# Performance work log

Hardware: AMD Instinct MI355X
Metric: run time of the kernel (lower is better)

The kernel has to match this reference:

```python
import jax, jax.numpy as jnp
import numpy as np

# Static config (matches init_kwargs)
VOCAB, EMBED, HIDDEN = 32000, 256, 512
SLOTS, MEM_DIM, HEADS, TOPK = 1024, 64, 4, 8
B, T = 16, 128
# beta_read/beta_write are learned scalars but the torch forward detaches them
# via .item(); treat as constants (|beta| + 1e-6 with beta init ~1.0).
BETA_R = 1.0 + 1e-6
BETA_W = 1.0 + 1e-6
EPS = 1e-8


def setup_inputs() -> dict:
    key = jax.random.key(0)
    ks = jax.random.split(key, 16)
    s = 0.02
    HD = HEADS * MEM_DIM
    return {
        "input_seq": jax.random.randint(ks[0], (B, T), 0, VOCAB),
        "E": jax.random.normal(ks[1], (VOCAB, EMBED), jnp.float32) * s,
        "W_ih": jax.random.normal(ks[2], (4 * HIDDEN, EMBED + MEM_DIM), jnp.float32) * s,
        "W_hh": jax.random.normal(ks[3], (4 * HIDDEN, HIDDEN), jnp.float32) * s,
        "b_ih": jnp.zeros((4 * HIDDEN,), jnp.float32),
        "b_hh": jnp.zeros((4 * HIDDEN,), jnp.float32),
        "W_out": jax.random.normal(ks[4], (HIDDEN, VOCAB), jnp.float32) * s,
        "b_out": jnp.zeros((VOCAB,), jnp.float32),
        "W_rk": jax.random.normal(ks[5], (HIDDEN, HD), jnp.float32) * s,
        "b_rk": jnp.zeros((HD,), jnp.float32),
        "W_wk": jax.random.normal(ks[6], (HIDDEN, HD), jnp.float32) * s,
        "b_wk": jnp.zeros((HD,), jnp.float32),
        "W_wv": jax.random.normal(ks[7], (HIDDEN, HD), jnp.float32) * s,
        "b_wv": jnp.zeros((HD,), jnp.float32),
        "W_er": jax.random.normal(ks[8], (HIDDEN, HD), jnp.float32) * s,
        "b_er": jnp.zeros((HD,), jnp.float32),
    }


def _address(memory, keys, beta):
    # memory: [B,S,D], keys: [B,H,D] -> sparse (top-k) content weights [B,H,S]
    mem_n = memory / (jnp.linalg.norm(memory, axis=-1, keepdims=True) + EPS)
    key_n = keys / (jnp.linalg.norm(keys, axis=-1, keepdims=True) + EPS)
    scores = beta * jnp.einsum("bhd,bsd->bhs", key_n, mem_n)
    vals, idx = jax.lax.top_k(scores, TOPK)           # [B,H,K]
    sm = jax.nn.softmax(vals, axis=-1)                # softmax over top-k only
    w = jnp.zeros_like(scores)
    b_ix = jnp.arange(scores.shape[0])[:, None, None]
    h_ix = jnp.arange(HEADS)[None, :, None]
    return w.at[b_ix, h_ix, idx].set(sm)              # [B,H,S]


def reference(input_seq, E, W_ih, W_hh, b_ih, b_hh, W_out, b_out,
              W_rk, b_rk, W_wk, b_wk, W_wv, b_wv, W_er, b_er):
    Bq = input_seq.shape[0]
    memory0 = jnp.full((Bq, SLOTS, MEM_DIM), 1e-6, jnp.float32)
    h0 = jnp.zeros((Bq, HIDDEN), jnp.float32)
    c0 = jnp.zeros((Bq, HIDDEN), jnp.float32)
    r0 = jnp.zeros((Bq, MEM_DIM), jnp.float32)

    def step(carry, x_t):
        memory, h, c, read_vec = carry
        emb = E[x_t]                                          # [B,embed]
        inp = jnp.concatenate([emb, read_vec], axis=-1)
        gates = inp @ W_ih.T + b_ih + h @ W_hh.T + b_hh       # [B,4H]
        i, f, g, o = jnp.split(gates, 4, axis=-1)             # torch LSTM order
        c = jax.nn.sigmoid(f) * c + jax.nn.sigmoid(i) * jnp.tanh(g)
        h = jax.nn.sigmoid(o) * jnp.tanh(c)
        logits = h @ W_out + b_out                            # [B,V]
        rk = (h @ W_rk + b_rk).reshape(Bq, HEADS, MEM_DIM)
        wk = (h @ W_wk + b_wk).reshape(Bq, HEADS, MEM_DIM)
        wv = (h @ W_wv + b_wv).reshape(Bq, HEADS, MEM_DIM)
        er = jax.nn.sigmoid(h @ W_er + b_er).reshape(Bq, HEADS, MEM_DIM)
        # content-addressed top-k read
        rw = _address(memory, rk, BETA_R)                     # [B,H,S]
        read_vec = jnp.einsum("bhs,bsd->bhd", rw, memory).mean(axis=1)
        # erase + add write
        ww = _address(memory, wk, BETA_W)                     # [B,H,S]
        keep = jnp.prod(1.0 - ww[..., None] * er[:, :, None, :], axis=1)
        add = jnp.einsum("bhs,bhd->bsd", ww, wv)
        memory = memory * keep + add
        return (memory, h, c, read_vec), logits

    _, logits_seq = jax.lax.scan(step, (memory0, h0, c0, r0), input_seq.T)
    return jnp.transpose(logits_seq, (1, 0, 2))               # [B,T,V]
```

## Files before the change

### kernel.cpp

```cpp
#include <hip/hip_runtime.h>
#include <hip/hip_bf16.h>
#include <stdint.h>

typedef unsigned int uint;
typedef unsigned long long u64;

#define T_STEPS 128
#define BQ 16
#define HID 512
#define NSLOT 1024
#define MD 64
#define VOCAB 32000
#define BETA 1.000001f
#define EPSN 1e-8f

#define NWK 128
#define NBT 16

#define LF_FH(b)  ((b)*32)
#define LF_FP(w)  ((16+(w))*32)
#define LF_FC(w)  ((48+(w))*32)
#define LF_FRV(b) ((176+(b))*32)
#define LF_FG(w)  ((192+(w))*32)
#define NLINES    320

#define AL4(dst, p) asm volatile("global_load_dwordx4 %0, %1, off sc0 sc1" : "=v"(dst) : "v"(p))
#define ALF(dst, p) asm volatile("global_load_dword %0, %1, off sc0 sc1" : "=v"(dst) : "v"(p))
#define AWAIT() do { asm volatile("s_waitcnt vmcnt(0)" ::: "memory"); __builtin_amdgcn_sched_barrier(0); } while(0)
#define DRAIN() asm volatile("s_waitcnt vmcnt(0)" ::: "memory")

__device__ __forceinline__ float sigm(float x){ return 1.f/(1.f+expf(-x)); }
__device__ __forceinline__ void astoref(float* p, float v){
  __hip_atomic_store(p, v, __ATOMIC_RELAXED, __HIP_MEMORY_SCOPE_AGENT);
}
__device__ __forceinline__ void astoreu32(uint* p, uint v){
  __hip_atomic_store(p, v, __ATOMIC_RELAXED, __HIP_MEMORY_SCOPE_AGENT);
}
__device__ __forceinline__ void astoreu64(u64* p, u64 v){
  __hip_atomic_store(p, v, __ATOMIC_RELAXED, __HIP_MEMORY_SCOPE_AGENT);
}
__device__ __forceinline__ u64 aloadu64(const u64* p){
  return __hip_atomic_load((u64*)p, __ATOMIC_RELAXED, __HIP_MEMORY_SCOPE_AGENT);
}
__device__ __forceinline__ uint aloadu32(const uint* p){
  return __hip_atomic_load((uint*)p, __ATOMIC_RELAXED, __HIP_MEMORY_SCOPE_AGENT);
}
__device__ __forceinline__ void poll1(const uint* p, uint gen){
  while (aloadu32(p) < gen) __builtin_amdgcn_s_sleep(2);
}

__device__ __forceinline__ u64 packsc(float v, int slot){
  uint u = __float_as_uint(v);
  u = (u & 0x80000000u) ? ~u : (u | 0x80000000u);
  return ((u64)u << 10) | (u64)(1023 - slot);
}
__device__ __forceinline__ float unpackval(u64 p){
  uint u = (uint)(p >> 10);
  uint bits = (u & 0x80000000u) ? (u & 0x7fffffffu) : ~u;
  return __uint_as_float(bits);
}
__device__ __forceinline__ int unpackslot(u64 p){ return 1023 - (int)(p & 1023u); }

#define L_MEM  0
#define L_NRM  8704
#define L_HS   8832
#define L_KEY  17088
#define L_KNRM 17600
#define L_SC   17608
#define L_WV   18632
#define L_ER   18888
#define L_WL   19144
#define L_RVS  19208
#define L_WTS  20232
#define L_TOT  21256

__global__ __launch_bounds__(256) void prep_emb(const float* __restrict__ E,
                                                const int* __restrict__ seq,
                                                float* __restrict__ EMB){
  int m = blockIdx.x, t = m >> 4, b = m & 15;
  int x = seq[b*T_STEPS + t];
  EMB[(size_t)m*256 + threadIdx.x] = E[(size_t)x*256 + threadIdx.x];
}

__global__ __launch_bounds__(256) void gemm_emb(const float* __restrict__ A,
                                                const float* __restrict__ W_ih,
                                                const float* __restrict__ b_ih,
                                                const float* __restrict__ b_hh,
                                                float* __restrict__ C){
  __shared__ __align__(16) float As[16*68];
  __shared__ __align__(16) float Bs[16*68];
  int mt = blockIdx.x & 31, nt = blockIdx.x >> 5;
  int m0 = mt*64, n0 = nt*64;
  int tx = threadIdx.x & 15, ty = threadIdx.x >> 4;
  float acc[4][4] = {};
  for (int k0 = 0; k0 < 256; k0 += 16){
    int mm = threadIdx.x >> 2, kq = (threadIdx.x & 3)*4;
    float4 a = *(const float4*)(A + (size_t)(m0+mm)*256 + k0 + kq);
    As[(kq+0)*68+mm]=a.x; As[(kq+1)*68+mm]=a.y; As[(kq+2)*68+mm]=a.z; As[(kq+3)*68+mm]=a.w;
    int pp = n0 + mm;
    int r = (pp & 3)*512 + (pp >> 2);
    float4 bv = *(const float4*)(W_ih + (size_t)r*320 + k0 + kq);
    Bs[(kq+0)*68+mm]=bv.x; Bs[(kq+1)*68+mm]=bv.y; Bs[(kq+2)*68+mm]=bv.z; Bs[(kq+3)*68+mm]=bv.w;
    __syncthreads();
    #pragma unroll
    for (int kk = 0; kk < 16; ++kk){
      float4 av = *(const float4*)(As + kk*68 + ty*4);
      float4 bb = *(const float4*)(Bs + kk*68 + tx*4);
      float aa[4] = {av.x,av.y,av.z,av.w};
      float bv2[4] = {bb.x,bb.y,bb.z,bb.w};
      #pragma unroll
      for (int i = 0; i < 4; ++i)
        #pragma unroll
        for (int j = 0; j < 4; ++j)
          acc[i][j] = fmaf(aa[i], bv2[j], acc[i][j]);
    }
    __syncthreads();
  }
  #pragma unroll
  for (int i = 0; i < 4; ++i){
    int m = m0 + ty*4 + i;
    #pragma unroll
    for (int j = 0; j < 4; ++j){
      int pp = n0 + tx*4 + j;
      int r = (pp & 3)*512 + (pp >> 2);
      C[(size_t)m*2048 + pp] = acc[i][j] + b_ih[r] + b_hh[r];
    }
  }
}

__global__ __launch_bounds__(256) void make_wrvT(const float* __restrict__ W_ih,
                                                 float* __restrict__ WT){
  int idx = blockIdx.x*256 + threadIdx.x;
  int k = idx >> 11, p = idx & 2047;
  int r = (p & 3)*512 + (p >> 2);
  WT[idx] = W_ih[(size_t)r*320 + 256 + k];
}

__global__ __launch_bounds__(256) void recur_kernel(
    const float* __restrict__ W_hh, const float* __restrict__ WT,
    const float* __restrict__ W_rk, const float* __restrict__ b_rk,
    const float* __restrict__ W_wk, const float* __restrict__ b_wk,
    const float* __restrict__ W_wv, const float* __restrict__ b_wv,
    const float* __restrict__ W_er, const float* __restrict__ b_er,
    const float* __restrict__ G_emb, float* __restrict__ H_all,
    float* __restrict__ H_pub, float* __restrict__ mem_g,
    float* __restrict__ projpub, float* __restrict__ gatespub,
    float* __restrict__ rvpub, u64* __restrict__ cand,
    u64* __restrict__ wlist, uint* __restrict__ arrv)
{
  __shared__ __align__(16) float smem[L_TOT];
  const int tid = threadIdx.x;
  const int wg  = blockIdx.x;

  if (wg < NWK){
    float* mem_s  = smem + L_MEM;
    float* nrm_s  = smem + L_NRM;
    float* hs     = smem + L_HS;
    float* key_s  = smem + L_KEY;
    float* knrm_s = smem + L_KNRM;
    float* sc_s   = smem + L_SC;
    float* wv_s   = smem + L_WV;
    float* er_s   = smem + L_ER;
    u64*   wl_s   = (u64*)(smem + L_WL);
    float* rv_s   = smem + L_RVS;
    float* WT_s   = smem + L_WTS;

    const int b_s = wg >> 3, rg = wg & 7, s0 = rg*128;
    const int gb = tid >> 4, gc = tid & 15;
    const int pcol = wg*16 + gc;
    const int rrow = (pcol & 3)*512 + (pcol >> 2);
    float* mslice_g = mem_g + ((size_t)b_s*NSLOT + s0)*MD;
    const float* W1 = (wg < 16) ? W_rk : W_wk;
    const float* B1 = (wg < 16) ? b_rk : b_wk;
    const float* W2 = (wg < 16) ? W_wv : W_er;
    const float* B2 = (wg < 16) ? b_wv : b_er;
    const int cc = (wg & 15)*16 + gc;
    const float pb1 = (wg < 32) ? B1[cc] : 0.f;
    const float pb2 = (wg < 32) ? B2[cc] : 0.f;

    for (int i = tid; i < 64*16; i += 256){
      int d = i >> 4, c = i & 15;
      WT_s[i] = WT[(size_t)d*2048 + wg*16 + c];
    }
    for (int i = tid; i < 128*MD; i += 256){
      mem_s[(i >> 6)*68 + (i & 63)] = 1e-6f;
      astoref(mslice_g + i, 1e-6f);
    }
    __syncthreads();
    {
      int s = tid >> 1, half = tid & 1;
      const float4* mp = (const float4*)(mem_s + s*68 + half*32);
      float sum = 0.f;
      #pragma unroll
      for (int q = 0; q < 8; ++q){
        float4 v = mp[q];
        sum = fmaf(v.x,v.x,sum); sum = fmaf(v.y,v.y,sum);
        sum = fmaf(v.z,v.z,sum); sum = fmaf(v.w,v.w,sum);
      }
      sum += __shfl_xor(sum, 1);
      if (half == 0) nrm_s[s] = sqrtf(sum) + EPSN;
    }
    __syncthreads();

    #pragma clang loop unroll(disable)
    for (int t = 0; t < T_STEPS-1; ++t){
      const int par = t & 1, parp = par ^ 1;
      if (t > 0){
        if (tid < 32) wl_s[tid] = aloadu64(wlist + (size_t)b_s*32 + tid);
        if (tid < 64){
          float4 v; AL4(v, (const float4*)(projpub + (size_t)parp*BQ*1024 + (size_t)b_s*1024 + 512) + tid);
          AWAIT();
          *(float4*)(wv_s + tid*4) = v;
        } else if (tid < 128){
          int i = tid - 64;
          float4 v; AL4(v, (const float4*)(projpub + (size_t)parp*BQ*1024 + (size_t)b_s*1024 + 768) + i);
          AWAIT();
          *(float4*)(er_s + i*4) = v;
        }
        __syncthreads();
        if (tid < 64){
          const int d = tid;
          #pragma unroll 1
          for (int e = 0; e < 32; ++e){
            u64 w64 = wl_s[e];
            int sl = (int)(w64 & 0xffffffffu);
            if (sl >= s0 && sl < s0+128){
              float w = __uint_as_float((uint)(w64 >> 32));
              mem_s[(sl-s0)*68 + d] *= (1.f - w*er_s[(e >> 3)*64 + d]);
            }
          }
          #pragma unroll 1
          for (int e = 0; e < 32; ++e){
            u64 w64 = wl_s[e];
            int sl = (int)(w64 & 0xffffffffu);
            if (sl >= s0 && sl < s0+128){
              float w = __uint_as_float((uint)(w64 >> 32));
              mem_s[(sl-s0)*68 + d] += w*wv_s[(e >> 3)*64 + d];
            }
          }
          #pragma unroll 1
          for (int e = 0; e < 32; ++e){
            u64 w64 = wl_s[e];
            int sl = (int)(w64 & 0xffffffffu);
            if (sl >= s0 && sl < s0+128)
              astoref(mslice_g + (sl-s0)*MD + d, mem_s[(sl-s0)*68 + d]);
          }
        }
        __syncthreads();
        {
          int s = tid >> 1, half = tid & 1;
          const float4* mp = (const float4*)(mem_s + s*68 + half*32);
          float sum = 0.f;
          #pragma unroll
          for (int q = 0; q < 8; ++q){
            float4 v = mp[q];
            sum = fmaf(v.x,v.x,sum); sum = fmaf(v.y,v.y,sum);
            sum = fmaf(v.z,v.z,sum); sum = fmaf(v.w,v.w,sum);
          }
          sum += __shfl_xor(sum, 1);
          if (half == 0) nrm_s[s] = sqrtf(sum) + EPSN;
        }
      }
      if (tid < 16) poll1(arrv + LF_FH(tid), (uint)(t+1));
      __syncthreads();
      {
        float4 v0,v1,v2,v3,v4,v5,v6,v7;
        const float4* hp = (const float4*)H_pub;
        AL4(v0, hp + tid);        AL4(v1, hp + tid + 256);
        AL4(v2, hp + tid + 512);  AL4(v3, hp + tid + 768);
        AL4(v4, hp + tid + 1024); AL4(v5, hp + tid + 1280);
        AL4(v6, hp + tid + 1536); AL4(v7, hp + tid + 1792);
        AWAIT();
        int i;
        i = tid;        *(float4*)(hs + (i>>7)*516 + (i&127)*4) = v0;
        i = tid + 256;  *(float4*)(hs + (i>>7)*516 + (i&127)*4) = v1;
        i = tid + 512;  *(float4*)(hs + (i>>7)*516 + (i&127)*4) = v2;
        i = tid + 768;  *(float4*)(hs + (i>>7)*516 + (i&127)*4) = v3;
        i = tid + 1024; *(float4*)(hs + (i>>7)*516 + (i&127)*4) = v4;
        i = tid + 1280; *(float4*)(hs + (i>>7)*516 + (i&127)*4) = v5;
        i = tid + 1536; *(float4*)(hs + (i>>7)*516 + (i&127)*4) = v6;
        i = tid + 1792; *(float4*)(hs + (i>>7)*516 + (i&127)*4) = v7;
      }
      __syncthreads();
      if (wg < 32){
        float a0=0.f,a1=0.f,b0=0.f,b1=0.f;
        const float* hp = hs + gb*516;
        const float* w1 = W1 + cc;
        const float* w2 = W2 + cc;
        #pragma unroll 4
        for (int k = 0; k < 512; k += 2){
          float h0 = hp[k], h1 = hp[k+1];
          a0 = fmaf(h0, w1[(size_t)k*256], a0);
          b0 = fmaf(h0, w2[(size_t)k*256], b0);
          a1 = fmaf(h1, w1[(size_t)(k+1)*256], a1);
          b1 = fmaf(h1, w2[(size_t)(k+1)*256], b1);
        }
        float v1 = a0 + a1 + pb1;
        float v2 = b0 + b1 + pb2;
        if (wg >= 16) v2 = sigm(v2);
        astoref(projpub + (size_t)par*BQ*1024 + (size_t)gb*1024 + wg*16 + gc, v1);
        astoref(projpub + (size_t)par*BQ*1024 + (size_t)gb*1024 + 512 + wg*16 + gc, v2);
      }
      DRAIN();
      __syncthreads();
      if (wg < 32 && tid == 0) astoreu32(arrv + LF_FP(wg), (uint)(t+1));
      if (tid < 32) poll1(arrv + LF_FP(tid), (uint)(t+1));
      __syncthreads();
      if (tid < 128){
        float4 kv; AL4(kv, (const float4*)(projpub + (size_t)par*BQ*1024 + (size_t)b_s*1024) + tid);
        AWAIT();
        *(float4*)(key_s + tid*4) = kv;
      }
      __syncthreads();
      if (tid < 8){
        const float4* kp = (const float4*)(key_s + tid*MD);
        float sum = 0.f;
        #pragma unroll
        for (int q = 0; q < 16; ++q){
          float4 v = kp[q];
          sum = fmaf(v.x,v.x,sum); sum = fmaf(v.y,v.y,sum);
          sum = fmaf(v.z,v.z,sum); sum = fmaf(v.w,v.w,sum);
        }
        knrm_s[tid] = sqrtf(sum) + EPSN;
      }
      __syncthreads();
      {
        int s = tid >> 1, kh = tid & 1;
        const float4* mp = (const float4*)(mem_s + s*68);
        float rnm = 1.f / nrm_s[s];
        float acc4[4] = {0.f,0.f,0.f,0.f};
        #pragma unroll
        for (int q = 0; q < 16; ++q){
          float4 m = mp[q];
          #pragma unroll
          for (int kk = 0; kk < 4; ++kk){
            float4 k4 = *(const float4*)(key_s + (kh*4+kk)*MD + q*4);
            acc4[kk] = fmaf(m.x,k4.x,acc4[kk]); acc4[kk] = fmaf(m.y,k4.y,acc4[kk]);
            acc4[kk] = fmaf(m.z,k4.z,acc4[kk]); acc4[kk] = fmaf(m.w,k4.w,acc4[kk]);
          }
        }
        #pragma unroll
        for (int kk = 0; kk < 4; ++kk){
          int key = kh*4 + kk;
          sc_s[key*128 + s] = BETA * acc4[kk] * rnm / knrm_s[key];
        }
      }
      __syncthreads();
      {
        int wid = tid >> 6, lane = tid & 63;
        #pragma unroll
        for (int kk = 0; kk < 2; ++kk){
          int key = wid*2 + kk;
          u64 p0 = packsc(sc_s[key*128 + lane],      s0 + lane);
          u64 p1 = packsc(sc_s[key*128 + 64 + lane], s0 + 64 + lane);
          #pragma unroll
          for (int r = 0; r < 8; ++r){
            u64 m = p0 > p1 ? p0 : p1;
            #pragma unroll
            for (int o = 32; o; o >>= 1){ u64 q = __shfl_xor(m, o); if (q > m) m = q; }
            if (p0 == m) p0 = 0; else if (p1 == m) p1 = 0;
            if (lane == 0) astoreu64(cand + (((size_t)b_s*8 + key)*8 + rg)*8 + r, m);
          }
        }
      }
      DRAIN();
      __syncthreads();
      if (tid == 0) astoreu32(arrv + LF_FC(wg), (uint)(t+1));
      float gpv;
      {
        float a0 = G_emb[(size_t)((t+1)*BQ + gb)*2048 + pcol];
        float a1 = 0.f, a2 = 0.f, a3 = 0.f;
        const float4* wh = (const float4*)(W_hh + (size_t)rrow*HID);
        const float4* xv = (const float4*)(hs + gb*516);
        #pragma unroll 2
        for (int k = 0; k < 128; k += 4){
          float4 w, x;
          w=wh[k+0]; x=xv[k+0]; a0=fmaf(w.x,x.x,a0); a0=fmaf(w.y,x.y,a0); a0=fmaf(w.z,x.z,a0); a0=fmaf(w.w,x.w,a0);
          w=wh[k+1]; x=xv[k+1]; a1=fmaf(w.x,x.x,a1); a1=fmaf(w.y,x.y,a1); a1=fmaf(w.z,x.z,a1); a1=fmaf(w.w,x.w,a1);
          w=wh[k+2]; x=xv[k+2]; a2=fmaf(w.x,x.x,a2); a2=fmaf(w.y,x.y,a2); a2=fmaf(w.z,x.z,a2); a2=fmaf(w.w,x.w,a2);
          w=wh[k+3]; x=xv[k+3]; a3=fmaf(w.x,x.x,a3); a3=fmaf(w.y,x.y,a3); a3=fmaf(w.z,x.z,a3); a3=fmaf(w.w,x.w,a3);
        }
        gpv = (a0+a1)+(a2+a3);
      }
      if (tid < 16) poll1(arrv + LF_FRV(tid), (uint)(t+1));
      __syncthreads();
      {
        float4 v; AL4(v, (const float4*)rvpub + tid); AWAIT();
        *(float4*)(rv_s + tid*4) = v;
      }
      __syncthreads();
      {
        float acc = gpv;
        #pragma unroll 8
        for (int d = 0; d < 64; ++d)
          acc = fmaf(rv_s[gb*64 + d], WT_s[d*16 + gc], acc);
        astoref(gatespub + (size_t)gb*2048 + pcol, acc);
      }
      DRAIN();
      __syncthreads();
      if (tid == 0) astoreu32(arrv + LF_FG(wg), (uint)(t+1));
    }
  } else {
    const int b = wg - NWK;
    float* rv_st = smem;
    float c0, c1;
    {
      float4 gA = *(const float4*)(G_emb + (size_t)b*2048 + tid*8);
      float4 gB = *(const float4*)(G_emb + (size_t)b*2048 + tid*8 + 4);
      c0 = sigm(gA.x)*tanhf(gA.z);
      float h0v = sigm(gA.w)*tanhf(c0);
      c1 = sigm(gB.x)*tanhf(gB.z);
      float h1v = sigm(gB.w)*tanhf(c1);
      astoref(H_pub + (size_t)b*HID + tid*2,     h0v);
      astoref(H_pub + (size_t)b*HID + tid*2 + 1, h1v);
      H_all[(size_t)b*HID + tid*2]     = h0v;
      H_all[(size_t)b*HID + tid*2 + 1] = h1v;
    }
    DRAIN();
    __syncthreads();
    if (tid == 0) astoreu32(arrv + LF_FH(b), 1u);

    #pragma clang loop unroll(disable)
    for (int t = 0; t < T_STEPS-1; ++t){
      if (tid < 8) poll1(arrv + LF_FC(b*8 + tid), (uint)(t+1));
      __syncthreads();
      {
        int wid = tid >> 6, lane = tid & 63;
        #pragma unroll
        for (int kk = 0; kk < 2; ++kk){
          int key = wid*2 + kk;
          u64 pv = aloadu64(cand + (((size_t)b*8 + key)*8 + (lane >> 3))*8 + (lane & 7));
          u64 sel = 0;
          #pragma unroll
          for (int r = 0; r < 8; ++r){
            u64 m = pv;
            #pragma unroll
            for (int o = 32; o; o >>= 1){ u64 q = __shfl_xor(m, o); if (q > m) m = q; }
            if (pv == m) pv = 0;
            if (lane == r) sel = m;
          }
          float val = unpackval(sel);
          int slot = unpackslot(sel);
          float vmax = __shfl(val, 0);
          float e = (lane < 8) ? expf(val - vmax) : 0.f;
          float ssum = e;
          #pragma unroll
          for (int o = 32; o; o >>= 1) ssum += __shfl_xor(ssum, o);
          float w = e / ssum;
          if (key < 4){
            int sls[8];
            #pragma unroll
            for (int i = 0; i < 8; ++i) sls[i] = __shfl(slot, i);
            float mv[8];
            #pragma unroll
            for (int i = 0; i < 8; ++i)
              ALF(mv[i], mem_g + ((size_t)b*NSLOT + sls[i])*MD + lane);
            AWAIT();
            float acc = 0.f;
            #pragma unroll
            for (int i = 0; i < 8; ++i) acc = fmaf(__shfl(w, i), mv[i], acc);
            rv_st[key*64 + lane] = acc;
          } else if (lane < 8){
            astoreu64(wlist + (size_t)b*32 + (key-4)*8 + lane,
                      ((u64)__float_as_uint(w) << 32) | (u64)(uint)slot);
          }
        }
      }
      __syncthreads();
      if (tid < 64){
        float m = 0.25f*(rv_st[tid] + rv_st[64+tid] + rv_st[128+tid] + rv_st[192+tid]);
        astoref(rvpub + (size_t)b*MD + tid, m);
      }
      DRAIN();
      __syncthreads();
      if (tid == 0) astoreu32(arrv + LF_FRV(b), (uint)(t+1));
      if (tid < 128) poll1(arrv + LF_FG(tid), (uint)(t+1));
      __syncthreads();
      {
        float4 gA, gB;
        AL4(gA, (const float4*)(gatespub + (size_t)b*2048) + tid*2);
        AL4(gB, (const float4*)(gatespub + (size_t)b*2048) + tid*2 + 1);
        AWAIT();
        c0 = sigm(gA.y)*c0 + sigm(gA.x)*tanhf(gA.z);
        float h0v = sigm(gA.w)*tanhf(c0);
        c1 = sigm(gB.y)*c1 + sigm(gB.x)*tanhf(gB.z);
        float h1v = sigm(gB.w)*tanhf(c1);
        astoref(H_pub + (size_t)b*HID + tid*2,     h0v);
        astoref(H_pub + (size_t)b*HID + tid*2 + 1, h1v);
        H_all[(size_t)((t+1)*BQ + b)*HID + tid*2]     = h0v;
        H_all[(size_t)((t+1)*BQ + b)*HID + tid*2 + 1] = h1v;
      }
      DRAIN();
      __syncthreads();
      if (tid == 0) astoreu32(arrv + LF_FH(b), (uint)(t+2));
    }
  }
}

__global__ __launch_bounds__(256) void gemm_out(const float* __restrict__ A,
                                                const float* __restrict__ Bmat,
                                                const float* __restrict__ bias,
                                                float* __restrict__ C){
  __shared__ __align__(16) float As[16*132];
  __shared__ __align__(16) float Bs[16*64];
  int mt = blockIdx.x & 15, nt = blockIdx.x >> 4;
  int m0 = mt*128, n0 = nt*64;
  int tx = threadIdx.x & 15, ty = threadIdx.x >> 4;
  float acc[8][4] = {};
  for (int k0 = 0; k0 < 512; k0 += 16){
    int mm = threadIdx.x >> 1, kq = (threadIdx.x & 1)*8;
    float4 a0 = *(const float4*)(A + (size_t)(m0+mm)*512 + k0 + kq);
    float4 a1 = *(const float4*)(A + (size_t)(m0+mm)*512 + k0 + kq + 4);
    As[(kq+0)*132+mm]=a0.x; As[(kq+1)*132+mm]=a0.y; As[(kq+2)*132+mm]=a0.z; As[(kq+3)*132+mm]=a0.w;
    As[(kq+4)*132+mm]=a1.x; As[(kq+5)*132+mm]=a1.y; As[(kq+6)*132+mm]=a1.z; As[(kq+7)*132+mm]=a1.w;
    int kk2 = threadIdx.x >> 4, nq = (threadIdx.x & 15)*4;
    *(float4*)(Bs + kk2*64 + nq) = *(const float4*)(Bmat + (size_t)(k0+kk2)*VOCAB + n0 + nq);
    __syncthreads();
    #pragma unroll
    for (int kk = 0; kk < 16; ++kk){
      float4 x0 = *(const float4*)(As + kk*132 + ty*8);
      float4 x1 = *(const float4*)(As + kk*132 + ty*8 + 4);
      float4 bv = *(const float4*)(Bs + kk*64 + tx*4);
      float aa[8] = {x0.x,x0.y,x0.z,x0.w,x1.x,x1.y,x1.z,x1.w};
      float bb[4] = {bv.x,bv.y,bv.z,bv.w};
      #pragma unroll
      for (int i = 0; i < 8; ++i)
        #pragma unroll
        for (int j = 0; j < 4; ++j)
          acc[i][j] = fmaf(aa[i], bb[j], acc[i][j]);
    }
    __syncthreads();
  }
  #pragma unroll
  for (int i = 0; i < 8; ++i){
    int m = m0 + ty*8 + i;
    int bq = m & 15, tt = m >> 4;
    float* crow = C + ((size_t)bq*T_STEPS + tt)*VOCAB + n0 + tx*4;
    #pragma unroll
    for (int j = 0; j < 4; ++j) crow[j] = acc[i][j] + bias[n0 + tx*4 + j];
  }
}

extern "C" void kernel_launch(void* const* d_in, const int* in_sizes, int n_in,
                              void* d_out, int out_size, void* d_ws, size_t ws_size,
                              hipStream_t stream){
  const int*   seq   = (const int*)d_in[0];
  const float* E     = (const float*)d_in[1];
  const float* W_ih  = (const float*)d_in[2];
  const float* W_hh  = (const float*)d_in[3];
  const float* b_ih  = (const float*)d_in[4];
  const float* b_hh  = (const float*)d_in[5];
  const float* W_out = (const float*)d_in[6];
  const float* b_out = (const float*)d_in[7];
  const float* W_rk  = (const float*)d_in[8];
  const float* b_rk  = (const float*)d_in[9];
  const float* W_wk  = (const float*)d_in[10];
  const float* b_wk  = (const float*)d_in[11];
  const float* W_wv  = (const float*)d_in[12];
  const float* b_wv  = (const float*)d_in[13];
  const float* W_er  = (const float*)d_in[14];
  const float* b_er  = (const float*)d_in[15];
  float* out = (float*)d_out;
  (void)in_sizes; (void)n_in; (void)out_size; (void)ws_size;

  char* ws = (char*)d_ws;
  size_t off = 0;
  auto alloc = [&](size_t bytes) -> void* {
    off = (off + 255) & ~(size_t)255;
    void* p = ws + off;
    off += bytes;
    return p;
  };
  float* EMB      = (float*)alloc((size_t)2048*256*4);
  float* G_emb    = (float*)alloc((size_t)2048*2048*4);
  float* H_all    = (float*)alloc((size_t)2048*512*4);
  float* H_pub    = (float*)alloc((size_t)16*512*4);
  float* mem_g    = (float*)alloc((size_t)16*1024*64*4);
  float* projpub  = (float*)alloc((size_t)2*16*1024*4);
  float* gatespub = (float*)alloc((size_t)16*2048*4);
  float* rvpub    = (float*)alloc((size_t)16*64*4);
  u64*   cand     = (u64*)alloc((size_t)16*8*8*8*8);
  u64*   wlist    = (u64*)alloc((size_t)16*32*8);
  float* WT       = (float*)alloc((size_t)64*2048*4);
  uint*  arrv     = (uint*)alloc((size_t)NLINES*32*4);

  hipMemsetAsync(arrv, 0, (size_t)NLINES*32*4, stream);
  prep_emb<<<2048, 256, 0, stream>>>(E, seq, EMB);
  gemm_emb<<<1024, 256, 0, stream>>>(EMB, W_ih, b_ih, b_hh, G_emb);
  make_wrvT<<<512, 256, 0, stream>>>(W_ih, WT);
  recur_kernel<<<NWK + NBT, 256, 0, stream>>>(
      W_hh, WT, W_rk, b_rk, W_wk, b_wk, W_wv, b_wv, W_er, b_er,
      G_emb, H_all, H_pub, mem_g, projpub, gatespub, rvpub, cand, wlist, arrv);
  gemm_out<<<16*500, 256, 0, stream>>>(H_all, W_out, b_out, out);
}
```

Baseline: 7.006 ms.

## Partition recurrence per batch row and sync via local 8-block groups

Restructures the persistent recurrent kernel so each batch row is owned by a group of 8 workgroups that handle memory slices, projections, top-k selection, read vector and LSTM gates. The 16 separate batch-tail workgroups and the global all-to-all gate barrier are removed, so flags now synchronize only within a row group. Projection weights are pre-transposed by a new kernel so the projections are computed per row group. Each workgroup now repeats the top-k merge and read redundantly, holds a larger WT slice in shared memory, and uses bounded polling loops that could silently time out.

```diff
diff --git a/kernel.cpp b/kernel.cpp
--- a/kernel.cpp
+++ b/kernel.cpp
@@ -14,15 +14,10 @@
 #define BETA 1.000001f
 #define EPSN 1e-8f
 
-#define NWK 128
-#define NBT 16
-
-#define LF_FH(b)  ((b)*32)
-#define LF_FP(w)  ((16+(w))*32)
-#define LF_FC(w)  ((48+(w))*32)
-#define LF_FRV(b) ((176+(b))*32)
-#define LF_FG(w)  ((192+(w))*32)
-#define NLINES    320
+#define LF_FH(b,o) (((b)*8+(o))*32)
+#define LF_FP(b,o) ((128+(b)*8+(o))*32)
+#define LF_FC(b,o) ((256+(b)*8+(o))*32)
+#define NLINES 384
 
 #define AL4(dst, p) asm volatile("global_load_dwordx4 %0, %1, off sc0 sc1" : "=v"(dst) : "v"(p))
 #define ALF(dst, p) asm volatile("global_load_dword %0, %1, off sc0 sc1" : "=v"(dst) : "v"(p))
@@ -45,8 +40,11 @@
 __device__ __forceinline__ uint aloadu32(const uint* p){
   return __hip_atomic_load((uint*)p, __ATOMIC_RELAXED, __HIP_MEMORY_SCOPE_AGENT);
 }
-__device__ __forceinline__ void poll1(const uint* p, uint gen){
-  while (aloadu32(p) < gen) __builtin_amdgcn_s_sleep(2);
+__device__ __forceinline__ void pollc(const uint* p, uint gen){
+  for (int i = 0; i < (1<<22); ++i){
+    if (aloadu32(p) >= gen) return;
+    __builtin_amdgcn_s_sleep(2);
+  }
 }
 
 __device__ __forceinline__ u64 packsc(float v, int slot){
@@ -61,18 +59,20 @@
 }
 __device__ __forceinline__ int unpackslot(u64 p){ return 1023 - (int)(p & 1023u); }
 
-#define L_MEM  0
-#define L_NRM  8704
-#define L_HS   8832
-#define L_KEY  17088
-#define L_KNRM 17600
-#define L_SC   17608
-#define L_WV   18632
-#define L_ER   18888
-#define L_WL   19144
-#define L_RVS  19208
-#define L_WTS  20232
-#define L_TOT  21256
+#define L_WT   0
+#define L_MEM  16384
+#define L_NRM  25088
+#define L_HS   25216
+#define L_KEY  25728
+#define L_SC   26240
+#define L_WV   27264
+#define L_ER   27520
+#define L_WL   27776
+#define L_GL   27840
+#define L_RVST 28096
+#define L_RVS  28352
+#define L_KN   28416
+#define L_TOT  28424
 
 __global__ __launch_bounds__(256) void prep_emb(const float* __restrict__ E,
                                                 const int* __restrict__ seq,
@@ -136,364 +136,331 @@
   WT[idx] = W_ih[(size_t)r*320 + 256 + k];
 }
 
-__global__ __launch_bounds__(256) void recur_kernel(
-    const float* __restrict__ W_hh, const float* __restrict__ WT,
-    const float* __restrict__ W_rk, const float* __restrict__ b_rk,
-    const float* __restrict__ W_wk, const float* __restrict__ b_wk,
-    const float* __restrict__ W_wv, const float* __restrict__ b_wv,
-    const float* __restrict__ W_er, const float* __restrict__ b_er,
+__global__ __launch_bounds__(256) void make_projT(const float* __restrict__ W_rk,
+                                                  const float* __restrict__ W_wk,
+                                                  const float* __restrict__ W_wv,
+                                                  const float* __restrict__ W_er,
+                                                  float* __restrict__ projT){
+  __shared__ float tl[32][33];
+  int bid = blockIdx.x;
+  int mt = bid >> 7, kt = (bid >> 3) & 15, ct = bid & 7;
+  const float* Wm = (mt==0)? W_rk : (mt==1)? W_wk : (mt==2)? W_wv : W_er;
+  int k0 = kt*32, c0 = ct*32;
+  int tx = threadIdx.x & 31, ty = threadIdx.x >> 5;
+  #pragma unroll
+  for (int i = 0; i < 4; ++i)
+    tl[ty + i*8][tx] = Wm[(size_t)(k0 + ty + i*8)*256 + c0 + tx];
+  __syncthreads();
+  #pragma unroll
+  for (int i = 0; i < 4; ++i)
+    projT[(size_t)(mt*256 + c0 + ty + i*8)*512 + k0 + tx] = tl[tx][ty + i*8];
+}
+
+__global__ __launch_bounds__(256, 1) void recur_kernel(
+    const float* __restrict__ W_hh,  const float* __restrict__ WT,
+    const float* __restrict__ projT, const float* __restrict__ b_rk,
+    const float* __restrict__ b_wk,  const float* __restrict__ b_wv,
+    const float* __restrict__ b_er,
     const float* __restrict__ G_emb, float* __restrict__ H_all,
-    float* __restrict__ H_pub, float* __restrict__ mem_g,
-    float* __restrict__ projpub, float* __restrict__ gatespub,
-    float* __restrict__ rvpub, u64* __restrict__ cand,
-    u64* __restrict__ wlist, uint* __restrict__ arrv)
+    float* __restrict__ h_pub, float* __restrict__ mem_g,
+    float* __restrict__ projpub, u64* __restrict__ cand,
+    uint* __restrict__ arrv)
 {
   __shared__ __align__(16) float smem[L_TOT];
+  float* WT_s   = smem + L_WT;
+  float* mem_s  = smem + L_MEM;
+  float* nrm_s  = smem + L_NRM;
+  float* hs     = smem + L_HS;
+  float* key_s  = smem + L_KEY;
+  float* sc_s   = smem + L_SC;
+  float* wv_s   = smem + L_WV;
+  float* er_s   = smem + L_ER;
+  u64*   wl_s   = (u64*)(smem + L_WL);
+  float* gl     = smem + L_GL;
+  float* rv_st  = smem + L_RVST;
+  float* rv_s   = smem + L_RVS;
+  float* knrm_s = smem + L_KN;
+
   const int tid = threadIdx.x;
   const int wg  = blockIdx.x;
-
-  if (wg < NWK){
-    float* mem_s  = smem + L_MEM;
-    float* nrm_s  = smem + L_NRM;
-    float* hs     = smem + L_HS;
-    float* key_s  = smem + L_KEY;
-    float* knrm_s = smem + L_KNRM;
-    float* sc_s   = smem + L_SC;
-    float* wv_s   = smem + L_WV;
-    float* er_s   = smem + L_ER;
-    u64*   wl_s   = (u64*)(smem + L_WL);
-    float* rv_s   = smem + L_RVS;
-    float* WT_s   = smem + L_WTS;
-
-    const int b_s = wg >> 3, rg = wg & 7, s0 = rg*128;
-    const int gb = tid >> 4, gc = tid & 15;
-    const int pcol = wg*16 + gc;
-    const int rrow = (pcol & 3)*512 + (pcol >> 2);
-    float* mslice_g = mem_g + ((size_t)b_s*NSLOT + s0)*MD;
-    const float* W1 = (wg < 16) ? W_rk : W_wk;
-    const float* B1 = (wg < 16) ? b_rk : b_wk;
-    const float* W2 = (wg < 16) ? W_wv : W_er;
-    const float* B2 = (wg < 16) ? b_wv : b_er;
-    const int cc = (wg & 15)*16 + gc;
-    const float pb1 = (wg < 32) ? B1[cc] : 0.f;
-    const float pb2 = (wg < 32) ? B2[cc] : 0.f;
-
-    for (int i = tid; i < 64*16; i += 256){
-      int d = i >> 4, c = i & 15;
-      WT_s[i] = WT[(size_t)d*2048 + wg*16 + c];
-    }
-    for (int i = tid; i < 128*MD; i += 256){
-      mem_s[(i >> 6)*68 + (i & 63)] = 1e-6f;
-      astoref(mslice_g + i, 1e-6f);
+  const int b   = wg >> 3, o = wg & 7;
+  const int s0  = o*128;
+  const int lane = tid & 63, wv_id = tid >> 6;
+  float* mslice_g = mem_g + ((size_t)b*NSLOT + s0)*MD;
+
+  const int cj = tid >> 1, phalf = tid & 1;
+  const int pp = o*128 + cj;
+  const int pms = pp >> 8, plc = pp & 255;
+  const float* pbv = (pms==0)? b_rk : (pms==1)? b_wk : (pms==2)? b_wv : b_er;
+  const float pbias = pbv[plc];
+  const int pcol = o*256 + tid;
+  const int rrow = (pcol & 3)*512 + (pcol >> 2);
+
+  for (int i = tid; i < 64*256; i += 256)
+    WT_s[i] = WT[(size_t)(i >> 8)*2048 + o*256 + (i & 255)];
+  for (int i = tid; i < 128*MD; i += 256){
+    mem_s[(i >> 6)*68 + (i & 63)] = 1e-6f;
+    astoref(mslice_g + i, 1e-6f);
+  }
+  __syncthreads();
+  {
+    int s = tid >> 1, half = tid & 1;
+    const float4* mp = (const float4*)(mem_s + s*68 + half*32);
+    float sum = 0.f;
+    #pragma unroll
+    for (int q = 0; q < 8; ++q){
+      float4 v = mp[q];
+      sum = fmaf(v.x,v.x,sum); sum = fmaf(v.y,v.y,sum);
+      sum = fmaf(v.z,v.z,sum); sum = fmaf(v.w,v.w,sum);
+    }
+    sum += __shfl_xor(sum, 1);
+    if (half == 0) nrm_s[s] = sqrtf(sum) + EPSN;
+  }
+  gl[tid] = G_emb[(size_t)b*2048 + pcol];
+  __syncthreads();
+  float c_reg = 0.f;
+  if (tid < 64){
+    float gi = gl[tid*4+0], gg = gl[tid*4+2], go = gl[tid*4+3];
+    c_reg = sigm(gi)*tanhf(gg);
+    float h = sigm(go)*tanhf(c_reg);
+    astoref(h_pub + (size_t)b*HID + o*64 + tid, h);
+    H_all[(size_t)b*HID + o*64 + tid] = h;
+  }
+  DRAIN();
+  __syncthreads();
+  if (tid == 0) astoreu32(arrv + LF_FH(b,o), 1u);
+
+  #pragma clang loop unroll(disable)
+  for (int t = 0; t < T_STEPS-1; ++t){
+    const int par = t & 1, parp = par ^ 1;
+    if (t > 0){
+      if (tid >= 4 && tid < 8) pollc(arrv + LF_FP(b, tid), (uint)t);
+      __syncthreads();
+      if (tid < 64){
+        float4 v; AL4(v, (const float4*)(projpub + (size_t)parp*BQ*1024 + (size_t)b*1024 + 512) + tid);
+        AWAIT();
+        *(float4*)(wv_s + tid*4) = v;
+      } else if (tid < 128){
+        int i = tid - 64;
+        float4 v; AL4(v, (const float4*)(projpub + (size_t)parp*BQ*1024 + (size_t)b*1024 + 768) + i);
+        AWAIT();
+        *(float4*)(er_s + i*4) = v;
+      }
+      __syncthreads();
+      if (tid < 64){
+        const int d = tid;
+        #pragma unroll 1
+        for (int e = 0; e < 32; ++e){
+          u64 w64 = wl_s[e];
+          int sl = (int)(w64 & 0xffffffffu);
+          if (sl >= s0 && sl < s0+128){
+            float w = __uint_as_float((uint)(w64 >> 32));
+            mem_s[(sl-s0)*68 + d] *= (1.f - w*er_s[(e >> 3)*64 + d]);
+          }
+        }
+        #pragma unroll 1
+        for (int e = 0; e < 32; ++e){
+          u64 w64 = wl_s[e];
+          int sl = (int)(w64 & 0xffffffffu);
+          if (sl >= s0 && sl < s0+128){
+            float w = __uint_as_float((uint)(w64 >> 32));
+            mem_s[(sl-s0)*68 + d] += w*wv_s[(e >> 3)*64 + d];
+          }
+        }
+        #pragma unroll 1
+        for (int e = 0; e < 32; ++e){
+          u64 w64 = wl_s[e];
+          int sl = (int)(w64 & 0xffffffffu);
+          if (sl >= s0 && sl < s0+128)
+            astoref(mslice_g + (sl-s0)*MD + d, mem_s[(sl-s0)*68 + d]);
+        }
+      }
+      __syncthreads();
+      {
+        int s = tid >> 1, half = tid & 1;
+        const float4* mp = (const float4*)(mem_s + s*68 + half*32);
+        float sum = 0.f;
+        #pragma unroll
+        for (int q = 0; q < 8; ++q){
+          float4 v = mp[q];
+          sum = fmaf(v.x,v.x,sum); sum = fmaf(v.y,v.y,sum);
+          sum = fmaf(v.z,v.z,sum); sum = fmaf(v.w,v.w,sum);
+        }
+        sum += __shfl_xor(sum, 1);
+        if (half == 0) nrm_s[s] = sqrtf(sum) + EPSN;
+      }
+    }
+    if (tid < 8) pollc(arrv + LF_FH(b, tid), (uint)(t+1));
+    __syncthreads();
+    if (tid < 128){
+      float4 v; AL4(v, (const float4*)h_pub + (size_t)b*128 + tid); AWAIT();
+      *(float4*)(hs + tid*4) = v;
     }
     __syncthreads();
     {
-      int s = tid >> 1, half = tid & 1;
-      const float4* mp = (const float4*)(mem_s + s*68 + half*32);
+      const float4* wp = (const float4*)(projT + (size_t)pp*512 + phalf*256);
+      const float4* xp = (const float4*)(hs + phalf*256);
+      float a0 = 0.f, a1 = 0.f;
+      #pragma unroll 4
+      for (int k = 0; k < 64; k += 2){
+        float4 w = wp[k], x = xp[k];
+        a0=fmaf(w.x,x.x,a0); a0=fmaf(w.y,x.y,a0); a0=fmaf(w.z,x.z,a0); a0=fmaf(w.w,x.w,a0);
+        w = wp[k+1]; x = xp[k+1];
+        a1=fmaf(w.x,x.x,a1); a1=fmaf(w.y,x.y,a1); a1=fmaf(w.z,x.z,a1); a1=fmaf(w.w,x.w,a1);
+      }
+      float acc = a0 + a1;
+      float other = __shfl_xor(acc, 1);
+      if (phalf == 0){
+        float v = acc + other + pbias;
+        if (pms == 3) v = sigm(v);
+        astoref(projpub + (size_t)par*BQ*1024 + (size_t)b*1024 + pp, v);
+      }
+    }
+    DRAIN();
+    __syncthreads();
+    if (tid == 0) astoreu32(arrv + LF_FP(b,o), (uint)(t+1));
+    if (tid < 4) pollc(arrv + LF_FP(b, tid), (uint)(t+1));
+    __syncthreads();
+    if (tid < 128){
+      float4 kv; AL4(kv, (const float4*)(projpub + (size_t)par*BQ*1024 + (size_t)b*1024) + tid);
+      AWAIT();
+      *(float4*)(key_s + tid*4) = kv;
+    }
+    __syncthreads();
+    if (tid < 8){
+      const float4* kp = (const float4*)(key_s + tid*MD);
       float sum = 0.f;
       #pragma unroll
-      for (int q = 0; q < 8; ++q){
-        float4 v = mp[q];
+      for (int q = 0; q < 16; ++q){
+        float4 v = kp[q];
         sum = fmaf(v.x,v.x,sum); sum = fmaf(v.y,v.y,sum);
         sum = fmaf(v.z,v.z,sum); sum = fmaf(v.w,v.w,sum);
       }
-      sum += __shfl_xor(sum, 1);
-      if (half == 0) nrm_s[s] = sqrtf(sum) + EPSN;
-    }
-    __syncthreads();
-
-    #pragma clang loop unroll(disable)
-    for (int t = 0; t < T_STEPS-1; ++t){
-      const int par = t & 1, parp = par ^ 1;
-      if (t > 0){
-        if (tid < 32) wl_s[tid] = aloadu64(wlist + (size_t)b_s*32 + tid);
-        if (tid < 64){
-          float4 v; AL4(v, (const float4*)(projpub + (size_t)parp*BQ*1024 + (size_t)b_s*1024 + 512) + tid);
+      knrm_s[tid] = sqrtf(sum) + EPSN;
+    }
+    __syncthreads();
+    {
+      int s = tid >> 1, kh = tid & 1;
+      const float4* mp = (const float4*)(mem_s + s*68);
+      float rnm = 1.f / nrm_s[s];
+      float acc4[4] = {0.f,0.f,0.f,0.f};
+      #pragma unroll
+      for (int q = 0; q < 16; ++q){
+        float4 m = mp[q];
+        #pragma unroll
+        for (int kk = 0; kk < 4; ++kk){
+          float4 k4 = *(const float4*)(key_s + (kh*4+kk)*MD + q*4);
+          acc4[kk] = fmaf(m.x,k4.x,acc4[kk]); acc4[kk] = fmaf(m.y,k4.y,acc4[kk]);
+          acc4[kk] = fmaf(m.z,k4.z,acc4[kk]); acc4[kk] = fmaf(m.w,k4.w,acc4[kk]);
+        }
+      }
+      #pragma unroll
+      for (int kk = 0; kk < 4; ++kk){
+        int key = kh*4 + kk;
+        sc_s[key*128 + s] = BETA * acc4[kk] * rnm / knrm_s[key];
+      }
+    }
+    __syncthreads();
+    {
+      #pragma unroll
+      for (int kk = 0; kk < 2; ++kk){
+        int key = wv_id*2 + kk;
+        u64 p0 = packsc(sc_s[key*128 + lane],      s0 + lane);
+        u64 p1 = packsc(sc_s[key*128 + 64 + lane], s0 + 64 + lane);
+        #pragma unroll
+        for (int r = 0; r < 8; ++r){
+          u64 m = p0 > p1 ? p0 : p1;
+          #pragma unroll
+          for (int oo = 32; oo; oo >>= 1){ u64 q = __shfl_xor(m, oo); if (q > m) m = q; }
+          if (p0 == m) p0 = 0; else if (p1 == m) p1 = 0;
+          if (lane == 0) astoreu64(cand + (((size_t)b*8 + key)*8 + o)*8 + r, m);
+        }
+      }
+    }
+    DRAIN();
+    __syncthreads();
+    if (tid == 0) astoreu32(arrv + LF_FC(b,o), (uint)(t+1));
+    float gpv;
+    {
+      float a0 = G_emb[(size_t)((t+1)*BQ + b)*2048 + pcol];
+      float a1 = 0.f, a2 = 0.f, a3 = 0.f;
+      const float4* wh = (const float4*)(W_hh + (size_t)rrow*HID);
+      const float4* xv = (const float4*)hs;
+      #pragma unroll 2
+      for (int k = 0; k < 128; k += 4){
+        float4 w, x;
+        w=wh[k+0]; x=xv[k+0]; a0=fmaf(w.x,x.x,a0); a0=fmaf(w.y,x.y,a0); a0=fmaf(w.z,x.z,a0); a0=fmaf(w.w,x.w,a0);
+        w=wh[k+1]; x=xv[k+1]; a1=fmaf(w.x,x.x,a1); a1=fmaf(w.y,x.y,a1); a1=fmaf(w.z,x.z,a1); a1=fmaf(w.w,x.w,a1);
+        w=wh[k+2]; x=xv[k+2]; a2=fmaf(w.x,x.x,a2); a2=fmaf(w.y,x.y,a2); a2=fmaf(w.z,x.z,a2); a2=fmaf(w.w,x.w,a2);
+        w=wh[k+3]; x=xv[k+3]; a3=fmaf(w.x,x.x,a3); a3=fmaf(w.y,x.y,a3); a3=fmaf(w.z,x.z,a3); a3=fmaf(w.w,x.w,a3);
+      }
+      gpv = (a0+a1)+(a2+a3);
+    }
+    if (tid < 8) pollc(arrv + LF_FC(b, tid), (uint)(t+1));
+    __syncthreads();
+    {
+      #pragma unroll
+      for (int kk = 0; kk < 2; ++kk){
+        int key = wv_id*2 + kk;
+        u64 pv = aloadu64(cand + (((size_t)b*8 + key)*8 + (lane >> 3))*8 + (lane & 7));
+        u64 sel = 0;
+        #pragma unroll
+        for (int r = 0; r < 8; ++r){
+          u64 m = pv;
+          #pragma unroll
+          for (int oo = 32; oo; oo >>= 1){ u64 q = __shfl_xor(m, oo); if (q > m) m = q; }
+          if (pv == m) pv = 0;
+          if (lane == r) sel = m;
+        }
+        float val = unpackval(sel);
+        int slot = unpackslot(sel);
+        float vmax = __shfl(val, 0);
+        float e = (lane < 8) ? expf(val - vmax) : 0.f;
+        float ssum = e;
+        #pragma unroll
+        for (int oo = 32; oo; oo >>= 1) ssum += __shfl_xor(ssum, oo);
+        float w = e / ssum;
+        if (key < 4){
+          int sls[8];
+          #pragma unroll
+          for (int i = 0; i < 8; ++i) sls[i] = __shfl(slot, i);
+          float mv[8];
+          #pragma unroll
+          for (int i = 0; i < 8; ++i)
+            ALF(mv[i], mem_g + ((size_t)b*NSLOT + sls[i])*MD + lane);
           AWAIT();
-          *(float4*)(wv_s + tid*4) = v;
-        } else if (tid < 128){
-          int i = tid - 64;
-          float4 v; AL4(v, (const float4*)(projpub + (size_t)parp*BQ*1024 + (size_t)b_s*1024 + 768) + i);
-          AWAIT();
-          *(float4*)(er_s + i*4) = v;
-        }
-        __syncthreads();
-        if (tid < 64){
-          const int d = tid;
-          #pragma unroll 1
-          for (int e = 0; e < 32; ++e){
-            u64 w64 = wl_s[e];
-            int sl = (int)(w64 & 0xffffffffu);
-            if (sl >= s0 && sl < s0+128){
-              float w = __uint_as_float((uint)(w64 >> 32));
-              mem_s[(sl-s0)*68 + d] *= (1.f - w*er_s[(e >> 3)*64 + d]);
-            }
-          }
-          #pragma unroll 1
-          for (int e = 0; e < 32; ++e){
-            u64 w64 = wl_s[e];
-            int sl = (int)(w64 & 0xffffffffu);
-            if (sl >= s0 && sl < s0+128){
-              float w = __uint_as_float((uint)(w64 >> 32));
-              mem_s[(sl-s0)*68 + d] += w*wv_s[(e >> 3)*64 + d];
-            }
-          }
-          #pragma unroll 1
-          for (int e = 0; e < 32; ++e){
-            u64 w64 = wl_s[e];
-            int sl = (int)(w64 & 0xffffffffu);
-            if (sl >= s0 && sl < s0+128)
-              astoref(mslice_g + (sl-s0)*MD + d, mem_s[(sl-s0)*68 + d]);
-          }
-        }
-        __syncthreads();
-        {
-          int s = tid >> 1, half = tid & 1;
-          const float4* mp = (const float4*)(mem_s + s*68 + half*32);
-          float sum = 0.f;
+          float acc = 0.f;
           #pragma unroll
-          for (int q = 0; q < 8; ++q){
-            float4 v = mp[q];
-            sum = fmaf(v.x,v.x,sum); sum = fmaf(v.y,v.y,sum);
-            sum = fmaf(v.z,v.z,sum); sum = fmaf(v.w,v.w,sum);
-          }
-          sum += __shfl_xor(sum, 1);
-          if (half == 0) nrm_s[s] = sqrtf(sum) + EPSN;
-        }
-      }
-      if (tid < 16) poll1(arrv + LF_FH(tid), (uint)(t+1));
-      __syncthreads();
-      {
-        float4 v0,v1,v2,v3,v4,v5,v6,v7;
-        const float4* hp = (const float4*)H_pub;
-        AL4(v0, hp + tid);        AL4(v1, hp + tid + 256);
-        AL4(v2, hp + tid + 512);  AL4(v3, hp + tid + 768);
-        AL4(v4, hp + tid + 1024); AL4(v5, hp + tid + 1280);
-        AL4(v6, hp + tid + 1536); AL4(v7, hp + tid + 1792);
-        AWAIT();
-        int i;
-        i = tid;        *(float4*)(hs + (i>>7)*516 + (i&127)*4) = v0;
-        i = tid + 256;  *(float4*)(hs + (i>>7)*516 + (i&127)*4) = v1;
-        i = tid + 512;  *(float4*)(hs + (i>>7)*516 + (i&127)*4) = v2;
-        i = tid + 768;  *(float4*)(hs + (i>>7)*516 + (i&127)*4) = v3;
-        i = tid + 1024; *(float4*)(hs + (i>>7)*516 + (i&127)*4) = v4;
-        i = tid + 1280; *(float4*)(hs + (i>>7)*516 + (i&127)*4) = v5;
-        i = tid + 1536; *(float4*)(hs + (i>>7)*516 + (i&127)*4) = v6;
-        i = tid + 1792; *(float4*)(hs + (i>>7)*516 + (i&127)*4) = v7;
-      }
-      __syncthreads();
-      if (wg < 32){
-        float a0=0.f,a1=0.f,b0=0.f,b1=0.f;
-        const float* hp = hs + gb*516;
-        const float* w1 = W1 + cc;
-        const float* w2 = W2 + cc;
-        #pragma unroll 4
-        for (int k = 0; k < 512; k += 2){
-          float h0 = hp[k], h1 = hp[k+1];
-          a0 = fmaf(h0, w1[(size_t)k*256], a0);
-          b0 = fmaf(h0, w2[(size_t)k*256], b0);
-          a1 = fmaf(h1, w1[(size_t)(k+1)*256], a1);
-          b1 = fmaf(h1, w2[(size_t)(k+1)*256], b1);
-        }
-        float v1 = a0 + a1 + pb1;
-        float v2 = b0 + b1 + pb2;
-        if (wg >= 16) v2 = sigm(v2);
-        astoref(projpub + (size_t)par*BQ*1024 + (size_t)gb*1024 + wg*16 + gc, v1);
-        astoref(projpub + (size_t)par*BQ*1024 + (size_t)gb*1024 + 512 + wg*16 + gc, v2);
-      }
-      DRAIN();
-      __syncthreads();
-      if (wg < 32 && tid == 0) astoreu32(arrv + LF_FP(wg), (uint)(t+1));
-      if (tid < 32) poll1(arrv + LF_FP(tid), (uint)(t+1));
-      __syncthreads();
-      if (tid < 128){
-        float4 kv; AL4(kv, (const float4*)(projpub + (size_t)par*BQ*1024 + (size_t)b_s*1024) + tid);
-        AWAIT();
-        *(float4*)(key_s + tid*4) = kv;
-      }
-      __syncthreads();
-      if (tid < 8){
-        const float4* kp = (const float4*)(key_s + tid*MD);
-        float sum = 0.f;
-        #pragma unroll
-        for (int q = 0; q < 16; ++q){
-          float4 v = kp[q];
-          sum = fmaf(v.x,v.x,sum); sum = fmaf(v.y,v.y,sum);
-          sum = fmaf(v.z,v.z,sum); sum = fmaf(v.w,v.w,sum);
-        }
-        knrm_s[tid] = sqrtf(sum) + EPSN;
-      }
-      __syncthreads();
-      {
-        int s = tid >> 1, kh = tid & 1;
-        const float4* mp = (const float4*)(mem_s + s*68);
-        float rnm = 1.f / nrm_s[s];
-        float acc4[4] = {0.f,0.f,0.f,0.f};
-        #pragma unroll
-        for (int q = 0; q < 16; ++q){
-          float4 m = mp[q];
-          #pragma unroll
-          for (int kk = 0; kk < 4; ++kk){
-            float4 k4 = *(const float4*)(key_s + (kh*4+kk)*MD + q*4);
-            acc4[kk] = fmaf(m.x,k4.x,acc4[kk]); acc4[kk] = fmaf(m.y,k4.y,acc4[kk]);
-            acc4[kk] = fmaf(m.z,k4.z,acc4[kk]); acc4[kk] = fmaf(m.w,k4.w,acc4[kk]);
-          }
-        }
-        #pragma unroll
-        for (int kk = 0; kk < 4; ++kk){
-          int key = kh*4 + kk;
-          sc_s[key*128 + s] = BETA * acc4[kk] * rnm / knrm_s[key];
-        }
-      }
-      __syncthreads();
-      {
-        int wid = tid >> 6, lane = tid & 63;
-        #pragma unroll
-        for (int kk = 0; kk < 2; ++kk){
-          int key = wid*2 + kk;
-          u64 p0 = packsc(sc_s[key*128 + lane],      s0 + lane);
-          u64 p1 = packsc(sc_s[key*128 + 64 + lane], s0 + 64 + lane);
-          #pragma unroll
-          for (int r = 0; r < 8; ++r){
-            u64 m = p0 > p1 ? p0 : p1;
-            #pragma unroll
-            for (int o = 32; o; o >>= 1){ u64 q = __shfl_xor(m, o); if (q > m) m = q; }
-            if (p0 == m) p0 = 0; else if (p1 == m) p1 = 0;
-            if (lane == 0) astoreu64(cand + (((size_t)b_s*8 + key)*8 + rg)*8 + r, m);
-          }
-        }
-      }
-      DRAIN();
-      __syncthreads();
-      if (tid == 0) astoreu32(arrv + LF_FC(wg), (uint)(t+1));
-      float gpv;
-      {
-        float a0 = G_emb[(size_t)((t+1)*BQ + gb)*2048 + pcol];
-        float a1 = 0.f, a2 = 0.f, a3 = 0.f;
-        const float4* wh = (const float4*)(W_hh + (size_t)rrow*HID);
-        const float4* xv = (const float4*)(hs + gb*516);
-        #pragma unroll 2
-        for (int k = 0; k < 128; k += 4){
-          float4 w, x;
-          w=wh[k+0]; x=xv[k+0]; a0=fmaf(w.x,x.x,a0); a0=fmaf(w.y,x.y,a0); a0=fmaf(w.z,x.z,a0); a0=fmaf(w.w,x.w,a0);
-          w=wh[k+1]; x=xv[k+1]; a1=fmaf(w.x,x.x,a1); a1=fmaf(w.y,x.y,a1); a1=fmaf(w.z,x.z,a1); a1=fmaf(w.w,x.w,a1);
-          w=wh[k+2]; x=xv[k+2]; a2=fmaf(w.x,x.x,a2); a2=fmaf(w.y,x.y,a2); a2=fmaf(w.z,x.z,a2); a2=fmaf(w.w,x.w,a2);
-          w=wh[k+3]; x=xv[k+3]; a3=fmaf(w.x,x.x,a3); a3=fmaf(w.y,x.y,a3); a3=fmaf(w.z,x.z,a3); a3=fmaf(w.w,x.w,a3);
-        }
-        gpv = (a0+a1)+(a2+a3);
-      }
-      if (tid < 16) poll1(arrv + LF_FRV(tid), (uint)(t+1));
-      __syncthreads();
-      {
-        float4 v; AL4(v, (const float4*)rvpub + tid); AWAIT();
-        *(float4*)(rv_s + tid*4) = v;
-      }
-      __syncthreads();
-      {
-        float acc = gpv;
-        #pragma unroll 8
-        for (int d = 0; d < 64; ++d)
-          acc = fmaf(rv_s[gb*64 + d], WT_s[d*16 + gc], acc);
-        astoref(gatespub + (size_t)gb*2048 + pcol, acc);
-      }
-      DRAIN();
-      __syncthreads();
-      if (tid == 0) astoreu32(arrv + LF_FG(wg), (uint)(t+1));
-    }
-  } else {
-    const int b = wg - NWK;
-    float* rv_st = smem;
-    float c0, c1;
+          for (int i = 0; i < 8; ++i) acc = fmaf(__shfl(w, i), mv[i], acc);
+          rv_st[key*64 + lane] = acc;
+        } else if (lane < 8){
+          wl_s[(key-4)*8 + lane] = ((u64)__float_as_uint(w) << 32) | (u64)(uint)slot;
+        }
+      }
+    }
+    __syncthreads();
+    if (tid < 64){
+      rv_s[tid] = 0.25f*(rv_st[tid] + rv_st[64+tid] + rv_st[128+tid] + rv_st[192+tid]);
+    }
+    __syncthreads();
     {
-      float4 gA = *(const float4*)(G_emb + (size_t)b*2048 + tid*8);
-      float4 gB = *(const float4*)(G_emb + (size_t)b*2048 + tid*8 + 4);
-      c0 = sigm(gA.x)*tanhf(gA.z);
-      float h0v = sigm(gA.w)*tanhf(c0);
-      c1 = sigm(gB.x)*tanhf(gB.z);
-      float h1v = sigm(gB.w)*tanhf(c1);
-      astoref(H_pub + (size_t)b*HID + tid*2,     h0v);
-      astoref(H_pub + (size_t)b*HID + tid*2 + 1, h1v);
-      H_all[(size_t)b*HID + tid*2]     = h0v;
-      H_all[(size_t)b*HID + tid*2 + 1] = h1v;
+      float acc = gpv;
+      #pragma unroll 8
+      for (int d = 0; d < 64; ++d)
+        acc = fmaf(rv_s[d], WT_s[d*256 + tid], acc);
+      gl[tid] = acc;
+    }
+    __syncthreads();
+    if (tid < 64){
+      float gi = gl[tid*4+0], gf = gl[tid*4+1], gg = gl[tid*4+2], go = gl[tid*4+3];
+      c_reg = sigm(gf)*c_reg + sigm(gi)*tanhf(gg);
+      float h = sigm(go)*tanhf(c_reg);
+      astoref(h_pub + (size_t)b*HID + o*64 + tid, h);
+      H_all[(size_t)((t+1)*BQ + b)*HID + o*64 + tid] = h;
     }
     DRAIN();
     __syncthreads();
-    if (tid == 0) astoreu32(arrv + LF_FH(b), 1u);
-
-    #pragma clang loop unroll(disable)
-    for (int t = 0; t < T_STEPS-1; ++t){
-      if (tid < 8) poll1(arrv + LF_FC(b*8 + tid), (uint)(t+1));
-      __syncthreads();
-      {
-        int wid = tid >> 6, lane = tid & 63;
-        #pragma unroll
-        for (int kk = 0; kk < 2; ++kk){
-          int key = wid*2 + kk;
-          u64 pv = aloadu64(cand + (((size_t)b*8 + key)*8 + (lane >> 3))*8 + (lane & 7));
-          u64 sel = 0;
-          #pragma unroll
-          for (int r = 0; r < 8; ++r){
-            u64 m = pv;
-            #pragma unroll
-            for (int o = 32; o; o >>= 1){ u64 q = __shfl_xor(m, o); if (q > m) m = q; }
-            if (pv == m) pv = 0;
-            if (lane == r) sel = m;
-          }
-          float val = unpackval(sel);
-          int slot = unpackslot(sel);
-          float vmax = __shfl(val, 0);
-          float e = (lane < 8) ? expf(val - vmax) : 0.f;
-          float ssum = e;
-          #pragma unroll
-          for (int o = 32; o; o >>= 1) ssum += __shfl_xor(ssum, o);
-          float w = e / ssum;
-          if (key < 4){
-            int sls[8];
-            #pragma unroll
-            for (int i = 0; i < 8; ++i) sls[i] = __shfl(slot, i);
-            float mv[8];
-            #pragma unroll
-            for (int i = 0; i < 8; ++i)
-              ALF(mv[i], mem_g + ((size_t)b*NSLOT + sls[i])*MD + lane);
-            AWAIT();
-            float acc = 0.f;
-            #pragma unroll
-            for (int i = 0; i < 8; ++i) acc = fmaf(__shfl(w, i), mv[i], acc);
-            rv_st[key*64 + lane] = acc;
-          } else if (lane < 8){
-            astoreu64(wlist + (size_t)b*32 + (key-4)*8 + lane,
-                      ((u64)__float_as_uint(w) << 32) | (u64)(uint)slot);
-          }
-        }
-      }
-      __syncthreads();
-      if (tid < 64){
-        float m = 0.25f*(rv_st[tid] + rv_st[64+tid] + rv_st[128+tid] + rv_st[192+tid]);
-        astoref(rvpub + (size_t)b*MD + tid, m);
-      }
-      DRAIN();
-      __syncthreads();
-      if (tid == 0) astoreu32(arrv + LF_FRV(b), (uint)(t+1));
-      if (tid < 128) poll1(arrv + LF_FG(tid), (uint)(t+1));
-      __syncthreads();
-      {
-        float4 gA, gB;
-        AL4(gA, (const float4*)(gatespub + (size_t)b*2048) + tid*2);
-        AL4(gB, (const float4*)(gatespub + (size_t)b*2048) + tid*2 + 1);
-        AWAIT();
-        c0 = sigm(gA.y)*c0 + sigm(gA.x)*tanhf(gA.z);
-        float h0v = sigm(gA.w)*tanhf(c0);
-        c1 = sigm(gB.y)*c1 + sigm(gB.x)*tanhf(gB.z);
-        float h1v = sigm(gB.w)*tanhf(c1);
-        astoref(H_pub + (size_t)b*HID + tid*2,     h0v);
-        astoref(H_pub + (size_t)b*HID + tid*2 + 1, h1v);
-        H_all[(size_t)((t+1)*BQ + b)*HID + tid*2]     = h0v;
-        H_all[(size_t)((t+1)*BQ + b)*HID + tid*2 + 1] = h1v;
-      }
-      DRAIN();
-      __syncthreads();
-      if (tid == 0) astoreu32(arrv + LF_FH(b), (uint)(t+2));
-    }
+    if (tid == 0) astoreu32(arrv + LF_FH(b,o), (uint)(t+2));
   }
 }
 
@@ -571,25 +538,24 @@
     off += bytes;
     return p;
   };
-  float* EMB      = (float*)alloc((size_t)2048*256*4);
-  float* G_emb    = (float*)alloc((size_t)2048*2048*4);
-  float* H_all    = (float*)alloc((size_t)2048*512*4);
-  float* H_pub    = (float*)alloc((size_t)16*512*4);
-  float* mem_g    = (float*)alloc((size_t)16*1024*64*4);
-  float* projpub  = (float*)alloc((size_t)2*16*1024*4);
-  float* gatespub = (float*)alloc((size_t)16*2048*4);
-  float* rvpub    = (float*)alloc((size_t)16*64*4);
-  u64*   cand     = (u64*)alloc((size_t)16*8*8*8*8);
-  u64*   wlist    = (u64*)alloc((size_t)16*32*8);
-  float* WT       = (float*)alloc((size_t)64*2048*4);
-  uint*  arrv     = (uint*)alloc((size_t)NLINES*32*4);
+  float* EMB     = (float*)alloc((size_t)2048*256*4);
+  float* G_emb   = (float*)alloc((size_t)2048*2048*4);
+  float* H_all   = (float*)alloc((size_t)2048*512*4);
+  float* h_pub   = (float*)alloc((size_t)16*512*4);
+  float* mem_g   = (float*)alloc((size_t)16*1024*64*4);
+  float* projpub = (float*)alloc((size_t)2*16*1024*4);
+  u64*   cand    = (u64*)alloc((size_t)16*8*8*8*8);
+  float* projT   = (float*)alloc((size_t)1024*512*4);
+  float* WT      = (float*)alloc((size_t)64*2048*4);
+  uint*  arrv    = (uint*)alloc((size_t)NLINES*32*4);
 
   hipMemsetAsync(arrv, 0, (size_t)NLINES*32*4, stream);
   prep_emb<<<2048, 256, 0, stream>>>(E, seq, EMB);
   gemm_emb<<<1024, 256, 0, stream>>>(EMB, W_ih, b_ih, b_hh, G_emb);
   make_wrvT<<<512, 256, 0, stream>>>(W_ih, WT);
-  recur_kernel<<<NWK + NBT, 256, 0, stream>>>(
-      W_hh, WT, W_rk, b_rk, W_wk, b_wk, W_wv, b_wv, W_er, b_er,
-      G_emb, H_all, H_pub, mem_g, projpub, gatespub, rvpub, cand, wlist, arrv);
+  make_projT<<<512, 256, 0, stream>>>(W_rk, W_wk, W_wv, W_er, projT);
+  recur_kernel<<<128, 256, 0, stream>>>(
+      W_hh, WT, projT, b_rk, b_wk, b_wv, b_er,
+      G_emb, H_all, h_pub, mem_g, projpub, cand, arrv);
   gemm_out<<<16*500, 256, 0, stream>>>(H_all, W_out, b_out, out);
 }
```

Result: slower. 7.185 ms (+2.6%).
